# Kernel optimization log

Hardware: AMD Instinct MI355X
Metric: run time of the kernel (lower is better)

Reference implementation:

```python
import jax, jax.numpy as jnp
import numpy as np
from jax import lax

N, C, H, W = 32, 256, 56, 56
SHIFT = 2  # p_5_1_0, frozen random.randint(-3,3)

def setup_inputs() -> dict:
    key = jax.random.key(0)
    k1, k2, k3 = jax.random.split(key, 3)
    x = jax.random.normal(k1, (N, C, H, W), dtype=jnp.float32)
    w6 = jax.random.normal(k2, (C, 1), dtype=jnp.float32) * 0.1  # trunc_normal(std=0.1) approx
    w7 = jax.random.normal(k3, (C, C * 25), dtype=jnp.float32) * (1.0 / np.sqrt(C * 25))
    return {"x": x, "w6": w6, "w7": w7}

def reference(x, w6, w7):
    # t_1: max over width -> (n,c,h)
    t1 = jnp.max(x, axis=3)
    # t_3/t_4: relu then tanh
    t4 = jnp.tanh(jax.nn.relu(x))
    # t_5: roll along height axis
    t5 = jnp.roll(x, SHIFT, axis=2)
    # t_6: einsum 'abcd,be->aecd' with e=1 -> (n,h,w)
    t6 = jnp.einsum('nchw,c->nhw', t4, w6[:, 0])
    # t_2 + p_7: unfold(5x5, dilation=3, padding=6) + 1x1 conv == dilated 5x5 conv.
    # unfold channel ordering is c*25 + (kh*5+kw), so reshape to OIHW directly.
    conv_w = w7.reshape(C, C, 5, 5)
    t7 = lax.conv_general_dilated(
        x, conv_w, window_strides=(1, 1), padding=[(6, 6), (6, 6)],
        rhs_dilation=(3, 3), dimension_numbers=('NCHW', 'OIHW', 'NCHW'))
    t8 = x * t7
    # t_9: softmax over width of (n,h,w)
    t9 = jax.nn.softmax(t6, axis=2)
    t10 = t9[:, None, :, :] * t5
    t11 = t10 + t8
    return t1[:, :, :, None] - t11
```

## Files before the change

### kernel.cpp

```cpp
#include <hip/hip_runtime.h>
#include <hip/hip_bf16.h>
#include <math.h>

typedef __bf16 bf16x8 __attribute__((ext_vector_type(8)));
typedef short  s16x8  __attribute__((ext_vector_type(8)));
typedef float  f32x4  __attribute__((ext_vector_type(4)));
typedef unsigned short u16;

#define NN 32
#define CC 256
#define HH 56
#define WW 56
#define HP 68
#define XP2_BYTES 75759616ull
#define XP2_OFF 0ull
#define WT3_OFF 75759616ull
#define T1_OFF  79036416ull
#define T9_OFF  80871424ull

__device__ inline u16 f2bf(float f) {
    unsigned int u = __builtin_bit_cast(unsigned int, f);
    u = (u + 0x7fffu + ((u >> 16) & 1u)) >> 16;
    return (u16)u;
}

__device__ inline void gl_lds16(const char* g, char* l) {
    __builtin_amdgcn_global_load_lds(
        (const __attribute__((address_space(1))) unsigned int*)g,
        (__attribute__((address_space(3))) unsigned int*)l, 16, 0, 0);
}

__global__ void zero_xp2(u16* __restrict__ xp2, size_t n16) {
    size_t i = (size_t)blockIdx.x * blockDim.x + threadIdx.x;
    size_t stride = (size_t)gridDim.x * blockDim.x;
    uint4* p = (uint4*)xp2;
    uint4 z; z.x = z.y = z.z = z.w = 0u;
    for (; i < n16; i += stride) p[i] = z;
}

__global__ __launch_bounds__(256)
void pack_x(const float* __restrict__ x, u16* __restrict__ xp2) {
    int nh = blockIdx.x;
    int n = nh / HH, h = nh % HH;
    int lane = threadIdx.x & 63, wv = threadIdx.x >> 6;
    if (lane >= WW) return;
    const float* src = x + (size_t)n * (CC * HH * WW) + h * WW + lane;
    u16* dst = xp2 + (((size_t)n * HP + (h + 6)) * HP + (lane + 6)) * CC;
    for (int oct = wv; oct < 32; oct += 4) {
        s16x8 pk;
#pragma unroll
        for (int j = 0; j < 8; ++j)
            pk[j] = (short)f2bf(src[(size_t)(oct * 8 + j) * (HH * WW)]);
        *(s16x8*)(dst + oct * 8) = pk;
    }
}

__global__ __launch_bounds__(256)
void pack_w(const float* __restrict__ w7, u16* __restrict__ wt3) {
    int idx = blockIdx.x * 256 + threadIdx.x;
    int c_out = idx / 6400;
    int k = idx - c_out * 6400;
    int cin = k / 25;
    int tap = k - cin * 25;
    int chunk = cin >> 5;
    int ci = cin & 31;
    wt3[(((size_t)(tap * 8 + chunk)) * CC + c_out) * 32 + ci] = f2bf(w7[idx]);
}

__global__ __launch_bounds__(256)
void t169_kernel(const float* __restrict__ x, const float* __restrict__ w6,
                 float* __restrict__ t1, float* __restrict__ t9) {
    const int n = blockIdx.x / HH;
    const int h = blockIdx.x % HH;
    const int wave = threadIdx.x >> 6;
    const int lane = threadIdx.x & 63;
    const bool valid = lane < WW;
    const int wl = valid ? lane : (WW - 1);
    const float* xrow = x + ((size_t)(n * CC) * HH + h) * WW;
    float accw = 0.f;
    __shared__ float sbuf[4 * 64];
    for (int i = 0; i < 64; ++i) {
        int c = wave * 64 + i;
        float xv = xrow[(size_t)c * (HH * WW) + wl];
        float xm = valid ? xv : -INFINITY;
#pragma unroll
        for (int off = 32; off > 0; off >>= 1)
            xm = fmaxf(xm, __shfl_xor(xm, off));
        if (lane == 0) t1[(size_t)(n * CC + c) * HH + h] = xm;
        if (valid) accw += tanhf(fmaxf(xv, 0.f)) * w6[c];
    }
    sbuf[wave * 64 + lane] = accw;
    __syncthreads();
    if (wave == 0) {
        float s = sbuf[lane] + sbuf[64 + lane] + sbuf[128 + lane] + sbuf[192 + lane];
        float sm = valid ? s : -INFINITY;
        float mx = sm;
#pragma unroll
        for (int off = 32; off > 0; off >>= 1)
            mx = fmaxf(mx, __shfl_xor(mx, off));
        float e = valid ? expf(s - mx) : 0.f;
        float tot = e;
#pragma unroll
        for (int off = 32; off > 0; off >>= 1)
            tot += __shfl_xor(tot, off);
        if (valid) t9[((size_t)n * HH + h) * WW + lane] = e / tot;
    }
}

__global__ __launch_bounds__(256, 3)
void conv_main(const char* __restrict__ xp2b, const char* __restrict__ wt3b,
               const float* __restrict__ x, const float* __restrict__ t1,
               const float* __restrict__ t9, float* __restrict__ out) {
    const int blk = blockIdx.x;
    const int g = blk & 1;
    const int tile = blk >> 1;
    const int tid = threadIdx.x;
    const int wid = tid >> 6;
    const int lane = tid & 63;
    const int m = lane & 15;
    const int q = lane >> 4;
    const int wgc = wid & 1;
    const int wgp = wid >> 1;

    __shared__ __align__(16) char smem[2][16384];

    const size_t aGoff = (size_t)g * 8192 + (size_t)wid * 4096 + (size_t)lane * 16;
    unsigned vb[4] = {0, 0, 0, 0};
    if (wid >= 2) {
#pragma unroll
        for (int i = 0; i < 4; ++i) {
            int p = tile * 128 + ((wid - 2) * 4 + i) * 16 + (lane >> 2);
            int n = p / (HH * WW);
            int rem = p - n * (HH * WW);
            int hh = rem / WW;
            int ww = rem - hh * WW;
            vb[i] = ((((unsigned)n * HP + hh + 6) * HP) + ww + 6) * 512 + (lane & 3) * 16;
        }
    }

    auto stage = [&](int kn, int nb) {
        char* dst = smem[nb];
        if (wid < 2) {
            const char* gsrc = wt3b + (size_t)kn * 16384 + aGoff;
            char* d = dst + wid * 4096 + lane * 16;
#pragma unroll
            for (int i = 0; i < 4; ++i) gl_lds16(gsrc + i * 1024, d + i * 1024);
        } else {
            const int tp = kn >> 3, ch = kn & 7;
            const ptrdiff_t tapoff =
                (ptrdiff_t)((tp / 5) * 3 - 6) * (HP * 512) +
                (ptrdiff_t)((tp % 5) * 3 - 6) * 512 + ch * 64;
            const char* gb = xp2b + tapoff;
            char* d = dst + 8192 + (wid - 2) * 4096 + lane * 16;
#pragma unroll
            for (int i = 0; i < 4; ++i) gl_lds16(gb + vb[i], d + i * 1024);
        }
    };

    f32x4 acc[4][4];
#pragma unroll
    for (int ct = 0; ct < 4; ++ct)
#pragma unroll
        for (int st = 0; st < 4; ++st) {
            acc[ct][st][0] = 0.f; acc[ct][st][1] = 0.f;
            acc[ct][st][2] = 0.f; acc[ct][st][3] = 0.f;
        }

    const int aOff = (wgc * 64 + m) * 64 + q * 16;
    const int bOff = 8192 + (wgp * 64 + m) * 64 + q * 16;

    stage(0, 0);
    for (int k = 0; k < 200; ++k) {
        __syncthreads();
        if (k < 199) stage(k + 1, (k + 1) & 1);
        const char* bp = smem[k & 1];
        bf16x8 av[4], bv[4];
#pragma unroll
        for (int ct = 0; ct < 4; ++ct)
            av[ct] = *(const bf16x8*)(const void*)(bp + aOff + ct * 1024);
#pragma unroll
        for (int st = 0; st < 4; ++st)
            bv[st] = *(const bf16x8*)(const void*)(bp + bOff + st * 1024);
#pragma unroll
        for (int ct = 0; ct < 4; ++ct)
#pragma unroll
            for (int st = 0; st < 4; ++st)
                acc[ct][st] = __builtin_amdgcn_mfma_f32_16x16x32_bf16(
                    av[ct], bv[st], acc[ct][st], 0, 0, 0);
    }

#pragma unroll
    for (int st = 0; st < 4; ++st) {
        const int p = tile * 128 + wgp * 64 + st * 16 + m;
        const int n = p / (HH * WW);
        const int rem = p - n * (HH * WW);
        const int h = rem / WW;
        const int w = rem - h * WW;
        const float t9v = t9[((size_t)n * HH + h) * WW + w];
        const int hprev = (h >= 2) ? (h - 2) : (h + HH - 2);
#pragma unroll
        for (int ct = 0; ct < 4; ++ct) {
            const int c = g * 128 + wgc * 64 + ct * 16 + q * 4;
#pragma unroll
            for (int r = 0; r < 4; ++r) {
                const size_t rowi = (size_t)(n * CC + c + r) * HH;
                const float t1v = t1[rowi + h];
                const float xv = x[(rowi + h) * WW + w];
                const float xr = x[(rowi + hprev) * WW + w];
                out[(rowi + h) * WW + w] = t1v - (t9v * xr + xv * acc[ct][st][r]);
            }
        }
    }
}

extern "C" void kernel_launch(void* const* d_in, const int* in_sizes, int n_in,
                              void* d_out, int out_size, void* d_ws, size_t ws_size,
                              hipStream_t stream) {
    const float* x  = (const float*)d_in[0];
    const float* w6 = (const float*)d_in[1];
    const float* w7 = (const float*)d_in[2];
    float* out = (float*)d_out;
    char* ws = (char*)d_ws;
    u16*   xp2 = (u16*)(ws + XP2_OFF);
    u16*   wt3 = (u16*)(ws + WT3_OFF);
    float* t1  = (float*)(ws + T1_OFF);
    float* t9  = (float*)(ws + T9_OFF);

    zero_xp2<<<dim3(2048), dim3(256), 0, stream>>>(xp2, XP2_BYTES / 16);
    pack_x<<<dim3(NN * HH), dim3(256), 0, stream>>>(x, xp2);
    pack_w<<<dim3(6400), dim3(256), 0, stream>>>(w7, wt3);
    t169_kernel<<<dim3(NN * HH), dim3(256), 0, stream>>>(x, w6, t1, t9);
    conv_main<<<dim3(1568), dim3(256), 0, stream>>>((const char*)xp2, (const char*)wt3,
                                                    x, t1, t9, out);
}
```

Baseline: 723.3 us.

## Fuse x packing into prep kernel, fragment-order LDS layout, XCD-aware tile mapping

```diff
diff --git a/kernel.cpp b/kernel.cpp
--- a/kernel.cpp
+++ b/kernel.cpp
@@ -14,7 +14,7 @@
 #define HP 68
 #define XP2_BYTES 75759616ull
 #define XP2_OFF 0ull
-#define WT3_OFF 75759616ull
+#define WT4_OFF 75759616ull
 #define T1_OFF  79036416ull
 #define T9_OFF  80871424ull
 
@@ -39,46 +39,34 @@
 }
 
 __global__ __launch_bounds__(256)
-void pack_x(const float* __restrict__ x, u16* __restrict__ xp2) {
-    int nh = blockIdx.x;
-    int n = nh / HH, h = nh % HH;
-    int lane = threadIdx.x & 63, wv = threadIdx.x >> 6;
-    if (lane >= WW) return;
-    const float* src = x + (size_t)n * (CC * HH * WW) + h * WW + lane;
-    u16* dst = xp2 + (((size_t)n * HP + (h + 6)) * HP + (lane + 6)) * CC;
-    for (int oct = wv; oct < 32; oct += 4) {
-        s16x8 pk;
-#pragma unroll
-        for (int j = 0; j < 8; ++j)
-            pk[j] = (short)f2bf(src[(size_t)(oct * 8 + j) * (HH * WW)]);
-        *(s16x8*)(dst + oct * 8) = pk;
-    }
-}
-
-__global__ __launch_bounds__(256)
-void pack_w(const float* __restrict__ w7, u16* __restrict__ wt3) {
+void pack_w(const float* __restrict__ w7, u16* __restrict__ wt4) {
     int idx = blockIdx.x * 256 + threadIdx.x;
     int c_out = idx / 6400;
-    int k = idx - c_out * 6400;
-    int cin = k / 25;
-    int tap = k - cin * 25;
-    int chunk = cin >> 5;
+    int k0 = idx - c_out * 6400;
+    int cin = k0 / 25;
+    int tap = k0 - cin * 25;
+    int k = tap * 8 + (cin >> 5);
     int ci = cin & 31;
-    wt3[(((size_t)(tap * 8 + chunk)) * CC + c_out) * 32 + ci] = f2bf(w7[idx]);
+    int q = ci >> 3, j = ci & 7;
+    int g = c_out >> 7, ch = (c_out >> 4) & 7, m = c_out & 15;
+    wt4[(((size_t)(k * 2 + g) * 8 + ch) * 64 + q * 16 + m) * 8 + j] = f2bf(w7[idx]);
 }
 
 __global__ __launch_bounds__(256)
-void t169_kernel(const float* __restrict__ x, const float* __restrict__ w6,
-                 float* __restrict__ t1, float* __restrict__ t9) {
+void prep(const float* __restrict__ x, const float* __restrict__ w6,
+          float* __restrict__ t1, float* __restrict__ t9, u16* __restrict__ xp2) {
     const int n = blockIdx.x / HH;
     const int h = blockIdx.x % HH;
-    const int wave = threadIdx.x >> 6;
-    const int lane = threadIdx.x & 63;
+    const int tid = threadIdx.x;
+    const int wave = tid >> 6;
+    const int lane = tid & 63;
     const bool valid = lane < WW;
     const int wl = valid ? lane : (WW - 1);
     const float* xrow = x + ((size_t)(n * CC) * HH + h) * WW;
+    __shared__ float sbuf[4 * 64];
+    __shared__ u16 tile[56 * 264];
     float accw = 0.f;
-    __shared__ float sbuf[4 * 64];
+    s16x8 pk;
     for (int i = 0; i < 64; ++i) {
         int c = wave * 64 + i;
         float xv = xrow[(size_t)c * (HH * WW) + wl];
@@ -88,6 +76,9 @@
             xm = fmaxf(xm, __shfl_xor(xm, off));
         if (lane == 0) t1[(size_t)(n * CC + c) * HH + h] = xm;
         if (valid) accw += tanhf(fmaxf(xv, 0.f)) * w6[c];
+        pk[i & 7] = (short)f2bf(xv);
+        if ((i & 7) == 7 && valid)
+            *(s16x8*)(tile + lane * 264 + (wave * 8 + (i >> 3)) * 8) = pk;
     }
     sbuf[wave * 64 + lane] = accw;
     __syncthreads();
@@ -105,15 +96,22 @@
             tot += __shfl_xor(tot, off);
         if (valid) t9[((size_t)n * HH + h) * WW + lane] = e / tot;
     }
+    u16* dst = xp2 + (((size_t)n * HP + (h + 6)) * HP + 6) * CC;
+    for (int g = tid; g < 56 * 32; g += 256) {
+        int w = g >> 5, cg = g & 31;
+        *(s16x8*)(dst + (size_t)w * CC + cg * 8) = *(const s16x8*)(tile + w * 264 + cg * 8);
+    }
 }
 
 __global__ __launch_bounds__(256, 3)
-void conv_main(const char* __restrict__ xp2b, const char* __restrict__ wt3b,
+void conv_main(const char* __restrict__ xp2b, const char* __restrict__ wt4b,
                const float* __restrict__ x, const float* __restrict__ t1,
                const float* __restrict__ t9, float* __restrict__ out) {
-    const int blk = blockIdx.x;
-    const int g = blk & 1;
-    const int tile = blk >> 1;
+    const int u = blockIdx.x;
+    const int xcd = u & 7;
+    const int i0 = u >> 3;
+    const int tile = xcd * 98 + (i0 >> 1);
+    const int g = i0 & 1;
     const int tid = threadIdx.x;
     const int wid = tid >> 6;
     const int lane = tid & 63;
@@ -124,24 +122,23 @@
 
     __shared__ __align__(16) char smem[2][16384];
 
-    const size_t aGoff = (size_t)g * 8192 + (size_t)wid * 4096 + (size_t)lane * 16;
     unsigned vb[4] = {0, 0, 0, 0};
     if (wid >= 2) {
 #pragma unroll
         for (int i = 0; i < 4; ++i) {
-            int p = tile * 128 + ((wid - 2) * 4 + i) * 16 + (lane >> 2);
+            int p = tile * 128 + ((wid - 2) * 4 + i) * 16 + (lane & 15);
             int n = p / (HH * WW);
             int rem = p - n * (HH * WW);
             int hh = rem / WW;
             int ww = rem - hh * WW;
-            vb[i] = ((((unsigned)n * HP + hh + 6) * HP) + ww + 6) * 512 + (lane & 3) * 16;
+            vb[i] = ((((unsigned)n * HP + hh + 6) * HP) + ww + 6) * 512 + (lane >> 4) * 16;
         }
     }
 
     auto stage = [&](int kn, int nb) {
         char* dst = smem[nb];
         if (wid < 2) {
-            const char* gsrc = wt3b + (size_t)kn * 16384 + aGoff;
+            const char* gsrc = wt4b + (size_t)(kn * 2 + g) * 8192 + wid * 4096 + lane * 16;
             char* d = dst + wid * 4096 + lane * 16;
 #pragma unroll
             for (int i = 0; i < 4; ++i) gl_lds16(gsrc + i * 1024, d + i * 1024);
@@ -166,8 +163,8 @@
             acc[ct][st][2] = 0.f; acc[ct][st][3] = 0.f;
         }
 
-    const int aOff = (wgc * 64 + m) * 64 + q * 16;
-    const int bOff = 8192 + (wgp * 64 + m) * 64 + q * 16;
+    const int aOff = wgc * 4096 + lane * 16;
+    const int bOff = 8192 + wgp * 4096 + lane * 16;
 
     stage(0, 0);
     for (int k = 0; k < 200; ++k) {
@@ -222,14 +219,13 @@
     float* out = (float*)d_out;
     char* ws = (char*)d_ws;
     u16*   xp2 = (u16*)(ws + XP2_OFF);
-    u16*   wt3 = (u16*)(ws + WT3_OFF);
+    u16*   wt4 = (u16*)(ws + WT4_OFF);
     float* t1  = (float*)(ws + T1_OFF);
     float* t9  = (float*)(ws + T9_OFF);
 
     zero_xp2<<<dim3(2048), dim3(256), 0, stream>>>(xp2, XP2_BYTES / 16);
-    pack_x<<<dim3(NN * HH), dim3(256), 0, stream>>>(x, xp2);
-    pack_w<<<dim3(6400), dim3(256), 0, stream>>>(w7, wt3);
-    t169_kernel<<<dim3(NN * HH), dim3(256), 0, stream>>>(x, w6, t1, t9);
-    conv_main<<<dim3(1568), dim3(256), 0, stream>>>((const char*)xp2, (const char*)wt3,
+    pack_w<<<dim3(6400), dim3(256), 0, stream>>>(w7, wt4);
+    prep<<<dim3(NN * HH), dim3(256), 0, stream>>>(x, w6, t1, t9, xp2);
+    conv_main<<<dim3(1568), dim3(256), 0, stream>>>((const char*)xp2, (const char*)wt4,
                                                     x, t1, t9, out);
 }
```

Measured after the change: 772.6 us. +6.8%, slower.
